# Kernel optimization log

Measured on AMD Instinct MI355X. Metric: run time of the kernel, lower is better.

## Reference

```python
import jax, jax.numpy as jnp
import numpy as np
import math

B, T, D, H = 2, 2048, 768, 12
ND = D // H  # head dim = 64


def precompute_freqs_cis(dim, end, theta=10000.0):
    freqs = 1.0 / (theta ** (jnp.arange(0, dim, 2, dtype=jnp.float32) / dim))  # [dim/2]
    t = jnp.arange(end, dtype=jnp.float32)
    freqs = jnp.outer(t, freqs)  # [end, dim/2]
    return jnp.cos(freqs), jnp.sin(freqs)


def apply_rotary_emb(q, k, cos, sin):
    # q, k: [b, t, h, nd]; cos/sin: [t, nd/2]
    def rot(x):
        xr, xi = x[..., 0::2], x[..., 1::2]  # even/odd interleaved split
        c = cos[None, :, None, :]
        s = sin[None, :, None, :]
        out_r = xr * c - xi * s
        out_i = xr * s + xi * c
        return jnp.stack([out_r, out_i], axis=-1).reshape(x.shape)
    return rot(q), rot(k)


def setup_inputs() -> dict:
    key = jax.random.key(0)
    ks = jax.random.split(key, 12)
    sc = 0.02
    q = jax.random.normal(ks[0], (B, T, D), dtype=jnp.float32)
    k = jax.random.normal(ks[1], (B, T, D), dtype=jnp.float32)
    v = jax.random.normal(ks[2], (B, T, D), dtype=jnp.float32)
    mask = jnp.tril(jnp.ones((T, T), dtype=jnp.int32))[None, None]  # causal [1,1,T,T]
    # weights stored as [d_in, d_out] (pre-transposed vs torch Linear)
    wq = jax.random.normal(ks[3], (D, D), dtype=jnp.float32) * sc
    bq = jax.random.normal(ks[4], (D,), dtype=jnp.float32) * sc
    wk = jax.random.normal(ks[5], (D, D), dtype=jnp.float32) * sc
    bk = jax.random.normal(ks[6], (D,), dtype=jnp.float32) * sc
    wv = jax.random.normal(ks[7], (D, D), dtype=jnp.float32) * sc
    bv = jax.random.normal(ks[8], (D,), dtype=jnp.float32) * sc
    wo = jax.random.normal(ks[9], (D, D), dtype=jnp.float32) * sc
    cos, sin = precompute_freqs_cis(ND, T)
    return {"q": q, "k": k, "v": v, "mask": mask, "wq": wq, "bq": bq,
            "wk": wk, "bk": bk, "wv": wv, "bv": bv, "wo": wo,
            "freqs_cos": cos, "freqs_sin": sin}


def reference(q, k, v, mask, wq, bq, wk, bk, wv, bv, wo, freqs_cos, freqs_sin):
    b, t, d = q.shape
    qh = (q @ wq + bq).reshape(b, t, H, ND)
    kh = (k @ wk + bk).reshape(b, t, H, ND)
    vh = (v @ wv + bv).reshape(b, t, H, ND).transpose(0, 2, 1, 3)  # [b,h,t,nd]
    qh, kh = apply_rotary_emb(qh, kh, freqs_cos[:t], freqs_sin[:t])
    qh = qh.transpose(0, 2, 1, 3)  # [b,h,t,nd]
    kh = kh.transpose(0, 2, 1, 3)
    attn = jnp.einsum('bhqd,bhkd->bhqk', qh, kh) / math.sqrt(ND)
    attn = jnp.where(mask == 0, jnp.float32(-jnp.inf), attn)
    probs = jax.nn.softmax(attn, axis=-1)
    out = jnp.einsum('bhqk,bhkd->bhqd', probs, vh)
    out = out.transpose(0, 2, 1, 3).reshape(b, t, d)
    return out @ wo
```

## Files before the change

### kernel.cpp

```cpp
#include <hip/hip_runtime.h>
#include <hip/hip_bf16.h>
#include <math.h>

#define BB 2
#define TT 2048
#define DD 768
#define HH 12
#define ND 64
#define MM (BB*TT)

typedef __attribute__((ext_vector_type(8))) short bf16x8;
typedef __attribute__((ext_vector_type(4))) float f32x4;
typedef __attribute__((ext_vector_type(16))) float f32x16;

__device__ __forceinline__ float bf2f(ushort u) {
    union { unsigned int i; float f; } v; v.i = ((unsigned int)u) << 16; return v.f;
}
__device__ __forceinline__ ushort f2bf(float f) {
    union { float f; unsigned int i; } v; v.f = f;
    unsigned int r = v.i + 0x7FFF + ((v.i >> 16) & 1);
    return (ushort)(r >> 16);
}

__device__ __forceinline__ void cp16(void* lds, const void* g) {
    __builtin_amdgcn_global_load_lds(
        (const __attribute__((address_space(1))) void*)g,
        (__attribute__((address_space(3))) void*)lds, 16, 0, 0);
}

__device__ __forceinline__ float fexp2(float x) {
    float r; asm("v_exp_f32 %0, %1" : "=v"(r) : "v"(x)); return r;
}
__device__ __forceinline__ unsigned int pk_bf16(float a, float b) {
    unsigned int r; asm("v_cvt_pk_bf16_f32 %0, %1, %2" : "=v"(r) : "v"(a), "v"(b)); return r;
}

__device__ __forceinline__ void plswap(unsigned int& a, unsigned int& b) {
#if __has_builtin(__builtin_amdgcn_permlane32_swap)
    auto r = __builtin_amdgcn_permlane32_swap(a, b, false, false);
    a = r[0]; b = r[1];
#else
    unsigned int sa = __shfl_xor((int)a, 32), sb = __shfl_xor((int)b, 32);
    bool hi = (threadIdx.x & 63) >= 32;
    unsigned int na = hi ? sb : a, nb = hi ? b : sa;
    a = na; b = nb;
#endif
}
__device__ __forceinline__ float partner32(float x, int hi) {
#if __has_builtin(__builtin_amdgcn_permlane32_swap)
    unsigned int u = __float_as_uint(x);
    auto r = __builtin_amdgcn_permlane32_swap(u, u, false, false);
    return __uint_as_float(hi ? r[0] : r[1]);
#else
    return __shfl_xor(x, 32);
#endif
}

#define QSCALE 0.18033688011112043f

__global__ void conv_x3(const float* __restrict__ x0, const float* __restrict__ x1,
                        const float* __restrict__ x2,
                        ushort* __restrict__ o0, ushort* __restrict__ o1,
                        ushort* __restrict__ o2)
{
    const float* x = blockIdx.z == 0 ? x0 : (blockIdx.z == 1 ? x1 : x2);
    ushort* o = blockIdx.z == 0 ? o0 : (blockIdx.z == 1 ? o1 : o2);
    int i = (blockIdx.x * 256 + threadIdx.x) * 4;
    if (i >= MM * DD) return;
    float4 v = *(const float4*)&x[i];
    ushort4 r;
    r.x = f2bf(v.x); r.y = f2bf(v.y); r.z = f2bf(v.z); r.w = f2bf(v.w);
    *(ushort4*)&o[i] = r;
}

__global__ __launch_bounds__(256) void conv_wT(const float* __restrict__ w0, const float* __restrict__ w1,
                        const float* __restrict__ w2, const float* __restrict__ w3,
                        ushort* __restrict__ o0, ushort* __restrict__ o1,
                        ushort* __restrict__ o2, ushort* __restrict__ o3)
{
    __shared__ ushort tile[64][72];
    const float* w = blockIdx.z == 0 ? w0 : blockIdx.z == 1 ? w1 : blockIdx.z == 2 ? w2 : w3;
    ushort* o = blockIdx.z == 0 ? o0 : blockIdx.z == 1 ? o1 : blockIdx.z == 2 ? o2 : o3;
    const int k0 = blockIdx.y * 64, n0 = blockIdx.x * 64;
    #pragma unroll
    for (int it = 0; it < 4; ++it) {
        int e = (threadIdx.x + it * 256) * 4;
        int r = e >> 6, c = e & 63;
        float4 v = *(const float4*)&w[(size_t)(k0 + r) * DD + n0 + c];
        tile[c + 0][r] = f2bf(v.x);
        tile[c + 1][r] = f2bf(v.y);
        tile[c + 2][r] = f2bf(v.z);
        tile[c + 3][r] = f2bf(v.w);
    }
    __syncthreads();
    #pragma unroll
    for (int it = 0; it < 4; ++it) {
        int e = (threadIdx.x + it * 256) * 4;
        int nr = e >> 6, kc = e & 63;
        ushort4 r4;
        r4.x = tile[nr][kc + 0];
        r4.y = tile[nr][kc + 1];
        r4.z = tile[nr][kc + 2];
        r4.w = tile[nr][kc + 3];
        *(ushort4*)&o[(size_t)(n0 + nr) * DD + k0 + kc] = r4;
    }
}

struct GArgs { const ushort* x; const ushort* wt; const float* bias; void* out;
               const float* cT; const float* sT; int rope; };

template<int MODE, int TM, int TN>
__global__ __launch_bounds__(256) void gemm_bf16(GArgs a0, GArgs a1, GArgs a2)
{
    constexpr int WM = TM / 2, WN = TN / 2;
    constexpr int MF = WM / 16, NF = WN / 16;
    constexpr int ABYTES = TM * 128;
    constexpr int BUFB = (TM + TN) * 128;
    constexpr int NPASS = BUFB / 4096;
    constexpr int NK = DD / 64;
    __shared__ __align__(16) ushort S[2][BUFB / 2];
    GArgs ga = (blockIdx.z == 0) ? a0 : (blockIdx.z == 1 ? a1 : a2);
    const int tid = threadIdx.x;
    const int w = tid >> 6, l = tid & 63;
    const int wr = w >> 1, wc = w & 1;
    const int n0 = blockIdx.x * TN, m0 = blockIdx.y * TM;

    f32x4 acc[MF][NF] = {};

    auto stage = [&](int buf, int k0) {
        #pragma unroll
        for (int it = 0; it < NPASS; ++it) {
            const int ob = it * 4096 + w * 1024;
            const int o = ob + l * 16;
            if (ob < ABYTES) {
                const int row = o >> 7, inner = o & 127;
                cp16((char*)&S[buf][0] + ob,
                     (const char*)ga.x + (size_t)(m0 + row) * (DD * 2) + k0 * 2 +
                     (inner ^ ((row & 7) << 4)));
            } else {
                const int o2 = o - ABYTES;
                const int row = o2 >> 7, inner = o2 & 127;
                cp16((char*)&S[buf][0] + ob,
                     (const char*)ga.wt + (size_t)(n0 + row) * (DD * 2) + k0 * 2 +
                     (inner ^ ((row & 7) << 4)));
            }
        }
    };

    stage(0, 0);
    __syncthreads();
    const int lq = l >> 4, lr = l & 15;
    for (int t = 0; t < NK; ++t) {
        const int cur = t & 1;
        if (t + 1 < NK) stage(cur ^ 1, (t + 1) * 64);
        const char* ab = (const char*)&S[cur][0];
        #pragma unroll
        for (int kc = 0; kc < 2; ++kc) {
            const int kb = kc * 64 + lq * 16;
            bf16x8 af[MF], bfr[NF];
            #pragma unroll
            for (int i = 0; i < MF; ++i) {
                const int row = WM * wr + 16 * i + lr;
                af[i] = *(const bf16x8*)(ab + row * 128 + (kb ^ ((row & 7) << 4)));
            }
            #pragma unroll
            for (int j = 0; j < NF; ++j) {
                const int row = WN * wc + 16 * j + lr;
                bfr[j] = *(const bf16x8*)(ab + ABYTES + row * 128 + (kb ^ ((row & 7) << 4)));
            }
            __builtin_amdgcn_s_setprio(1);
            #pragma unroll
            for (int i = 0; i < MF; ++i)
                #pragma unroll
                for (int j = 0; j < NF; ++j)
                    acc[i][j] = __builtin_amdgcn_mfma_f32_16x16x32_bf16(af[i], bfr[j], acc[i][j], 0, 0, 0);
            __builtin_amdgcn_s_setprio(0);
        }
        __syncthreads();
    }

    #pragma unroll
    for (int i = 0; i < MF; ++i) {
        #pragma unroll
        for (int j = 0; j < NF; ++j) {
            #pragma unroll
            for (int r = 0; r < 4; ++r) {
                const int m = m0 + WM * wr + 16 * i + (l >> 4) * 4 + r;
                const int n = n0 + WN * wc + 16 * j + (l & 15);
                float v = acc[i][j][r];
                if (MODE == 0) {
                    v += ga.bias[n];
                    const int tt = m & 2047;
                    if (ga.rope) {
                        const int d = n & 63;
                        const float c = ga.cT[tt * 32 + (d >> 1)];
                        const float s = ga.sT[tt * 32 + (d >> 1)];
                        const float pv = __shfl_xor(v, 1);
                        v = (n & 1) ? (pv * s + v * c) : (v * c - pv * s);
                        if (ga.rope == 2) v *= QSCALE;
                    }
                    const int b = m >> 11;
                    const int h = n >> 6, d = n & 63;
                    ((ushort*)ga.out)[((size_t)(b * HH + h) * TT + tt) * ND + d] = f2bf(v);
                } else {
                    ((float*)ga.out)[(size_t)m * DD + n] = v;
                }
            }
        }
    }
}

__global__ __launch_bounds__(256) void transpose_v(const ushort* __restrict__ Vh,
                                                   ushort* __restrict__ VhT)
{
    __shared__ ushort tile[64][72];
    const int t0 = blockIdx.x * 64, bh = blockIdx.y;
    const ushort* src = Vh + ((size_t)bh * TT + t0) * ND;
    #pragma unroll
    for (int it = 0; it < 4; ++it) {
        int e = (threadIdx.x + it * 256) * 4;
        int r = e >> 6, c = e & 63;
        ushort4 v = *(const ushort4*)&src[r * ND + c];
        tile[r][c + 0] = v.x; tile[r][c + 1] = v.y;
        tile[r][c + 2] = v.z; tile[r][c + 3] = v.w;
    }
    __syncthreads();
    #pragma unroll
    for (int it = 0; it < 4; ++it) {
        int e = (threadIdx.x + it * 256) * 4;
        int d = e >> 6, tc = e & 63;
        ushort4 r4;
        r4.x = tile[tc + 0][d]; r4.y = tile[tc + 1][d];
        r4.z = tile[tc + 2][d]; r4.w = tile[tc + 3][d];
        *(ushort4*)&VhT[((size_t)bh * ND + d) * TT + t0 + tc] = r4;
    }
}

#define NQB (TT/128)
#define NBH (BB*HH)
#define NTASK (NQB*NBH)
#define NCU 256

__global__ __launch_bounds__(512) void attn_mfma4(const ushort* __restrict__ Qh,
                                                  const ushort* __restrict__ Kh,
                                                  const ushort* __restrict__ VhT,
                                                  ushort* __restrict__ Op)
{
    __shared__ __align__(16) ushort Ks[2][2][4096];
    __shared__ __align__(16) ushort Vs[2][2][4096];
    const int tid = threadIdx.x;
    const int w = tid >> 6, l = tid & 63;
    const int lq = l & 31, hi = l >> 5;
    const int qs = w & 3;
    const int kvh = w >> 2;

    const int n = blockIdx.x;
    const int r_ = (n < NCU) ? n : (NTASK - 1 + NCU - n);
    const int qblk = (NQB - 1) - r_ / NBH;
    const int bh = r_ % NBH;

    const int q0 = qblk * 128;
    const int q0w = q0 + qs * 32;
    const int qg = q0w + lq;
    const int ntH = qblk + 1;
    const int kvbase = kvh * ntH * 64;

    const ushort* Qg = Qh + ((size_t)bh * TT + q0w) * ND;
    const ushort* Kg = Kh + (size_t)bh * TT * ND;
    const ushort* Vg = VhT + (size_t)bh * ND * TT;

    bf16x8 qf[4];
    #pragma unroll
    for (int ks = 0; ks < 4; ++ks)
        qf[ks] = *(const bf16x8*)((const char*)Qg + lq * 128 + ks * 32 + hi * 16);

    auto stageKV = [&](int buf, int kv0) {
        #pragma unroll
        for (int it = 0; it < 2; ++it) {
            int o = it * 4096 + qs * 1024 + l * 16;
            int row = o >> 7, inner = o & 127;
            int swz = inner ^ ((row & 7) << 4);
            cp16((char*)&Ks[kvh][buf][0] + it * 4096 + qs * 1024,
                 (const char*)Kg + (size_t)(kv0 + row) * 128 + swz);
            cp16((char*)&Vs[kvh][buf][0] + it * 4096 + qs * 1024,
                 (const char*)Vg + (size_t)row * (TT * 2) + kv0 * 2 + swz);
        }
    };

    float m = -1e30f, lsum = 0.f;
    f32x16 o0 = {}, o1 = {};

    stageKV(0, kvbase);
    __syncthreads();
    for (int t = 0; t < ntH; ++t) {
        const int cur = t & 1;
        if (t + 1 < ntH) stageKV(cur ^ 1, kvbase + (t + 1) * 64);
        const char* kb = (const char*)&Ks[kvh][cur][0];
        const char* vb = (const char*)&Vs[kvh][cur][0];
        const int kvt = kvbase + t * 64;

        if (kvt <= q0w + 31) {
            const bool have1 = (kvt + 32 <= q0w + 31);

            f32x16 st0 = {}, st1 = {};
            __builtin_amdgcn_s_setprio(1);
            #pragma unroll
            for (int ks = 0; ks < 4; ++ks) {
                bf16x8 kf = *(const bf16x8*)(kb + lq * 128 +
                                             ((ks * 32 + hi * 16) ^ ((lq & 7) << 4)));
                st0 = __builtin_amdgcn_mfma_f32_32x32x16_bf16(kf, qf[ks], st0, 0, 0, 0);
            }
            if (have1) {
                #pragma unroll
                for (int ks = 0; ks < 4; ++ks) {
                    bf16x8 kf = *(const bf16x8*)(kb + (32 + lq) * 128 +
                                                 ((ks * 32 + hi * 16) ^ ((lq & 7) << 4)));
                    st1 = __builtin_amdgcn_mfma_f32_32x32x16_bf16(kf, qf[ks], st1, 0, 0, 0);
                }
            }
            __builtin_amdgcn_s_setprio(0);

            float tm = -1e30f;
            if (kvt + 31 > q0w) {
                #pragma unroll
                for (int r = 0; r < 16; ++r) {
                    const int kvg = kvt + (r & 3) + 8 * (r >> 2) + 4 * hi;
                    float x = (kvg <= qg) ? st0[r] : -1e30f;
                    st0[r] = x;
                    tm = fmaxf(tm, x);
                }
            } else {
                #pragma unroll
                for (int r = 0; r < 16; ++r) tm = fmaxf(tm, st0[r]);
            }
            if (have1) {
                if (kvt + 63 > q0w) {
                    #pragma unroll
                    for (int r = 0; r < 16; ++r) {
                        const int kvg = kvt + 32 + (r & 3) + 8 * (r >> 2) + 4 * hi;
                        float x = (kvg <= qg) ? st1[r] : -1e30f;
                        st1[r] = x;
                        tm = fmaxf(tm, x);
                    }
                } else {
                    #pragma unroll
                    for (int r = 0; r < 16; ++r) tm = fmaxf(tm, st1[r]);
                }
            }
            tm = fmaxf(tm, partner32(tm, hi));

            const bool defer = __all(tm <= m + 11.5f);
            float alpha = 1.f;
            if (!defer) {
                const float nm = fmaxf(m, tm);
                alpha = fexp2(m - nm);
                m = nm;
            }

            float ps[16];
            unsigned int pkA[8], pkB[8];
            #pragma unroll
            for (int i = 0; i < 8; ++i) {
                const float p0 = fexp2(st0[2 * i + 0] - m);
                const float p1 = fexp2(st0[2 * i + 1] - m);
                pkA[i] = pk_bf16(p0, p1);
                ps[i] = p0 + p1;
            }
            if (have1) {
                #pragma unroll
                for (int i = 0; i < 8; ++i) {
                    const float p0 = fexp2(st1[2 * i + 0] - m);
                    const float p1 = fexp2(st1[2 * i + 1] - m);
                    pkB[i] = pk_bf16(p0, p1);
                    ps[8 + i] = p0 + p1;
                }
            } else {
                #pragma unroll
                for (int i = 0; i < 8; ++i) { pkB[i] = 0; ps[8 + i] = 0.f; }
            }
            const float t0s = (ps[0] + ps[1]) + (ps[2] + ps[3]);
            const float t1s = (ps[4] + ps[5]) + (ps[6] + ps[7]);
            const float t2s = (ps[8] + ps[9]) + (ps[10] + ps[11]);
            const float t3s = (ps[12] + ps[13]) + (ps[14] + ps[15]);
            float rs = (t0s + t1s) + (t2s + t3s);
            rs += partner32(rs, hi);
            lsum = lsum * alpha + rs;

            plswap(pkA[0], pkA[2]); plswap(pkA[1], pkA[3]);
            plswap(pkA[4], pkA[6]); plswap(pkA[5], pkA[7]);
            if (have1) {
                plswap(pkB[0], pkB[2]); plswap(pkB[1], pkB[3]);
                plswap(pkB[4], pkB[6]); plswap(pkB[5], pkB[7]);
            }
            union { unsigned int u[4]; bf16x8 v; } pa0, pa1, pa2, pa3;
            pa0.u[0] = pkA[0]; pa0.u[1] = pkA[1]; pa0.u[2] = pkA[2]; pa0.u[3] = pkA[3];
            pa1.u[0] = pkA[4]; pa1.u[1] = pkA[5]; pa1.u[2] = pkA[6]; pa1.u[3] = pkA[7];
            pa2.u[0] = pkB[0]; pa2.u[1] = pkB[1]; pa2.u[2] = pkB[2]; pa2.u[3] = pkB[3];
            pa3.u[0] = pkB[4]; pa3.u[1] = pkB[5]; pa3.u[2] = pkB[6]; pa3.u[3] = pkB[7];

            if (!defer) {
                #pragma unroll
                for (int r = 0; r < 16; ++r) { o0[r] *= alpha; o1[r] *= alpha; }
            }

            __builtin_amdgcn_s_setprio(1);
            #pragma unroll
            for (int sl = 0; sl < 2; ++sl) {
                const bf16x8 pf = sl == 0 ? pa0.v : pa1.v;
                const int cb = sl * 32 + hi * 16;
                bf16x8 va = *(const bf16x8*)(vb + lq * 128 + (cb ^ ((lq & 7) << 4)));
                bf16x8 vc = *(const bf16x8*)(vb + (lq + 32) * 128 + (cb ^ ((lq & 7) << 4)));
                o0 = __builtin_amdgcn_mfma_f32_32x32x16_bf16(va, pf, o0, 0, 0, 0);
                o1 = __builtin_amdgcn_mfma_f32_32x32x16_bf16(vc, pf, o1, 0, 0, 0);
            }
            if (have1) {
                #pragma unroll
                for (int sl = 0; sl < 2; ++sl) {
                    const bf16x8 pf = sl == 0 ? pa2.v : pa3.v;
                    const int cb = 64 + sl * 32 + hi * 16;
                    bf16x8 va = *(const bf16x8*)(vb + lq * 128 + (cb ^ ((lq & 7) << 4)));
                    bf16x8 vc = *(const bf16x8*)(vb + (lq + 32) * 128 + (cb ^ ((lq & 7) << 4)));
                    o0 = __builtin_amdgcn_mfma_f32_32x32x16_bf16(va, pf, o0, 0, 0, 0);
                    o1 = __builtin_amdgcn_mfma_f32_32x32x16_bf16(vc, pf, o1, 0, 0, 0);
                }
            }
            __builtin_amdgcn_s_setprio(0);
        }
        __syncthreads();
    }

    float* xO  = (float*)&Ks[0][0][0];
    float* xML = (float*)&Vs[0][0][0];
    if (kvh == 1) {
        float* dst = xO + qs * 2048;
        #pragma unroll
        for (int r = 0; r < 16; ++r) {
            dst[r * 64 + l] = o0[r];
            dst[(r + 16) * 64 + l] = o1[r];
        }
        if (hi == 0) { xML[qs * 64 + lq] = m; xML[qs * 64 + 32 + lq] = lsum; }
    }
    __syncthreads();
    if (kvh == 0) {
        const float* src = xO + qs * 2048;
        const float m1 = xML[qs * 64 + lq];
        const float l1 = xML[qs * 64 + 32 + lq];
        const float ms = fmaxf(m, m1);
        const float a0 = fexp2(m - ms), a1 = fexp2(m1 - ms);
        const float inv = 1.0f / (lsum * a0 + l1 * a1);
        const int b = bh / HH, h = bh % HH;
        ushort* dst = Op + ((size_t)(b * TT + qg)) * DD + h * ND;
        #pragma unroll
        for (int g = 0; g < 4; ++g) {
            ushort4 w0, w1;
            w0.x = f2bf((o0[4 * g + 0] * a0 + src[(4 * g + 0) * 64 + l] * a1) * inv);
            w0.y = f2bf((o0[4 * g + 1] * a0 + src[(4 * g + 1) * 64 + l] * a1) * inv);
            w0.z = f2bf((o0[4 * g + 2] * a0 + src[(4 * g + 2) * 64 + l] * a1) * inv);
            w0.w = f2bf((o0[4 * g + 3] * a0 + src[(4 * g + 3) * 64 + l] * a1) * inv);
            *(ushort4*)&dst[8 * g + 4 * hi] = w0;
            w1.x = f2bf((o1[4 * g + 0] * a0 + src[(16 + 4 * g + 0) * 64 + l] * a1) * inv);
            w1.y = f2bf((o1[4 * g + 1] * a0 + src[(16 + 4 * g + 1) * 64 + l] * a1) * inv);
            w1.z = f2bf((o1[4 * g + 2] * a0 + src[(16 + 4 * g + 2) * 64 + l] * a1) * inv);
            w1.w = f2bf((o1[4 * g + 3] * a0 + src[(16 + 4 * g + 3) * 64 + l] * a1) * inv);
            *(ushort4*)&dst[32 + 8 * g + 4 * hi] = w1;
        }
    }
}

extern "C" void kernel_launch(void* const* d_in, const int* in_sizes, int n_in,
                              void* d_out, int out_size, void* d_ws, size_t ws_size,
                              hipStream_t stream)
{
    const float* q  = (const float*)d_in[0];
    const float* k  = (const float*)d_in[1];
    const float* v  = (const float*)d_in[2];
    const float* wq = (const float*)d_in[4];
    const float* bq = (const float*)d_in[5];
    const float* wk = (const float*)d_in[6];
    const float* bk = (const float*)d_in[7];
    const float* wv = (const float*)d_in[8];
    const float* bv = (const float*)d_in[9];
    const float* wo = (const float*)d_in[10];
    const float* fc = (const float*)d_in[11];
    const float* fs = (const float*)d_in[12];
    float* out = (float*)d_out;

    ushort* qB  = (ushort*)d_ws;
    ushort* kB  = qB  + (size_t)MM * DD;
    ushort* vB  = kB  + (size_t)MM * DD;
    ushort* wqT = vB  + (size_t)MM * DD;
    ushort* wkT = wqT + (size_t)DD * DD;
    ushort* wvT = wkT + (size_t)DD * DD;
    ushort* woT = wvT + (size_t)DD * DD;
    ushort* Qh  = woT + (size_t)DD * DD;
    ushort* Kh  = Qh  + (size_t)MM * DD;
    ushort* Vh  = Kh  + (size_t)MM * DD;
    ushort* VhT = kB;
    ushort* Op  = qB;

    conv_x3<<<dim3(MM * DD / 4 / 256, 1, 3), 256, 0, stream>>>(q, k, v, qB, kB, vB);
    conv_wT<<<dim3(DD / 64, DD / 64, 4), 256, 0, stream>>>(wq, wk, wv, wo, wqT, wkT, wvT, woT);

    GArgs aq{qB, wqT, bq, (void*)Qh, fc, fs, 2};
    GArgs ak{kB, wkT, bk, (void*)Kh, fc, fs, 1};
    GArgs av{vB, wvT, bv, (void*)Vh, nullptr, nullptr, 0};
    gemm_bf16<0, 128, 64><<<dim3(DD / 64, MM / 128, 3), 256, 0, stream>>>(aq, ak, av);

    transpose_v<<<dim3(TT / 64, BB * HH), 256, 0, stream>>>(Vh, VhT);

    attn_mfma4<<<dim3(NTASK), 512, 0, stream>>>(Qh, Kh, VhT, Op);

    GArgs ao{Op, woT, nullptr, (void*)out, nullptr, nullptr, 0};
    gemm_bf16<1, 64, 64><<<dim3(DD / 64, MM / 64, 1), 256, 0, stream>>>(ao, ao, ao);
}
```

Measured before the change: 105.1 us.

## Fuse V transpose into projection GEMM epilogue and merge conversion kernels

The V projection GEMM now stages its bias-added bf16 tile in shared memory and writes it directly in the transposed [b,h,d,t] layout the attention kernel reads. This removes the separate transpose_v kernel and its extra global round trip. The input and weight conversion kernels are merged into one grid-strided launch to cut launch overhead. The costs are an extra LDS pass and a barrier in the V epilogue, plus idle blocks in the weight slices of the merged grid.

Result: faster. 99.23 us (-5.6%).

```diff
diff --git a/kernel.cpp b/kernel.cpp
--- a/kernel.cpp
+++ b/kernel.cpp
@@ -58,51 +58,55 @@
 
 #define QSCALE 0.18033688011112043f
 
-__global__ void conv_x3(const float* __restrict__ x0, const float* __restrict__ x1,
-                        const float* __restrict__ x2,
-                        ushort* __restrict__ o0, ushort* __restrict__ o1,
-                        ushort* __restrict__ o2)
+__global__ __launch_bounds__(256) void conv_all(
+    const float* __restrict__ x0, const float* __restrict__ x1, const float* __restrict__ x2,
+    ushort* __restrict__ o0, ushort* __restrict__ o1, ushort* __restrict__ o2,
+    const float* __restrict__ w0, const float* __restrict__ w1,
+    const float* __restrict__ w2, const float* __restrict__ w3,
+    ushort* __restrict__ t0, ushort* __restrict__ t1,
+    ushort* __restrict__ t2, ushort* __restrict__ t3)
 {
-    const float* x = blockIdx.z == 0 ? x0 : (blockIdx.z == 1 ? x1 : x2);
-    ushort* o = blockIdx.z == 0 ? o0 : (blockIdx.z == 1 ? o1 : o2);
-    int i = (blockIdx.x * 256 + threadIdx.x) * 4;
-    if (i >= MM * DD) return;
-    float4 v = *(const float4*)&x[i];
-    ushort4 r;
-    r.x = f2bf(v.x); r.y = f2bf(v.y); r.z = f2bf(v.z); r.w = f2bf(v.w);
-    *(ushort4*)&o[i] = r;
-}
-
-__global__ __launch_bounds__(256) void conv_wT(const float* __restrict__ w0, const float* __restrict__ w1,
-                        const float* __restrict__ w2, const float* __restrict__ w3,
-                        ushort* __restrict__ o0, ushort* __restrict__ o1,
-                        ushort* __restrict__ o2, ushort* __restrict__ o3)
-{
-    __shared__ ushort tile[64][72];
-    const float* w = blockIdx.z == 0 ? w0 : blockIdx.z == 1 ? w1 : blockIdx.z == 2 ? w2 : w3;
-    ushort* o = blockIdx.z == 0 ? o0 : blockIdx.z == 1 ? o1 : blockIdx.z == 2 ? o2 : o3;
-    const int k0 = blockIdx.y * 64, n0 = blockIdx.x * 64;
-    #pragma unroll
-    for (int it = 0; it < 4; ++it) {
-        int e = (threadIdx.x + it * 256) * 4;
-        int r = e >> 6, c = e & 63;
-        float4 v = *(const float4*)&w[(size_t)(k0 + r) * DD + n0 + c];
-        tile[c + 0][r] = f2bf(v.x);
-        tile[c + 1][r] = f2bf(v.y);
-        tile[c + 2][r] = f2bf(v.z);
-        tile[c + 3][r] = f2bf(v.w);
-    }
-    __syncthreads();
-    #pragma unroll
-    for (int it = 0; it < 4; ++it) {
-        int e = (threadIdx.x + it * 256) * 4;
-        int nr = e >> 6, kc = e & 63;
-        ushort4 r4;
-        r4.x = tile[nr][kc + 0];
-        r4.y = tile[nr][kc + 1];
-        r4.z = tile[nr][kc + 2];
-        r4.w = tile[nr][kc + 3];
-        *(ushort4*)&o[(size_t)(n0 + nr) * DD + k0 + kc] = r4;
+    const int z = blockIdx.z;
+    if (z < 3) {
+        const float* x = z == 0 ? x0 : (z == 1 ? x1 : x2);
+        ushort* o = z == 0 ? o0 : (z == 1 ? o1 : o2);
+        const int total4 = MM * DD / 4;
+        for (int i = blockIdx.x * 256 + threadIdx.x; i < total4; i += gridDim.x * 256) {
+            float4 v = *(const float4*)&x[i * 4];
+            ushort4 r;
+            r.x = f2bf(v.x); r.y = f2bf(v.y); r.z = f2bf(v.z); r.w = f2bf(v.w);
+            *(ushort4*)&o[i * 4] = r;
+        }
+    } else {
+        if (blockIdx.x >= (DD / 64) * (DD / 64)) return;
+        __shared__ ushort tile[64][72];
+        const int zz = z - 3;
+        const float* w = zz == 0 ? w0 : zz == 1 ? w1 : zz == 2 ? w2 : w3;
+        ushort* o = zz == 0 ? t0 : zz == 1 ? t1 : zz == 2 ? t2 : t3;
+        const int n0 = (blockIdx.x % (DD / 64)) * 64;
+        const int k0 = (blockIdx.x / (DD / 64)) * 64;
+        #pragma unroll
+        for (int it = 0; it < 4; ++it) {
+            int e = (threadIdx.x + it * 256) * 4;
+            int r = e >> 6, c = e & 63;
+            float4 v = *(const float4*)&w[(size_t)(k0 + r) * DD + n0 + c];
+            tile[c + 0][r] = f2bf(v.x);
+            tile[c + 1][r] = f2bf(v.y);
+            tile[c + 2][r] = f2bf(v.z);
+            tile[c + 3][r] = f2bf(v.w);
+        }
+        __syncthreads();
+        #pragma unroll
+        for (int it = 0; it < 4; ++it) {
+            int e = (threadIdx.x + it * 256) * 4;
+            int nr = e >> 6, kc = e & 63;
+            ushort4 r4;
+            r4.x = tile[nr][kc + 0];
+            r4.y = tile[nr][kc + 1];
+            r4.z = tile[nr][kc + 2];
+            r4.w = tile[nr][kc + 3];
+            *(ushort4*)&o[(size_t)(n0 + nr) * DD + k0 + kc] = r4;
+        }
     }
 }
 
@@ -179,6 +183,33 @@
         __syncthreads();
     }
 
+    if (MODE == 0 && ga.rope == -1) {
+        ushort* tl = (ushort*)&S[0][0];
+        #pragma unroll
+        for (int i = 0; i < MF; ++i) {
+            #pragma unroll
+            for (int j = 0; j < NF; ++j) {
+                #pragma unroll
+                for (int r = 0; r < 4; ++r) {
+                    const int ml = WM * wr + 16 * i + (l >> 4) * 4 + r;
+                    const int nl = WN * wc + 16 * j + (l & 15);
+                    tl[nl * (TM + 8) + ml] = f2bf(acc[i][j][r] + ga.bias[n0 + nl]);
+                }
+            }
+        }
+        __syncthreads();
+        const int b = m0 >> 11, t0b = m0 & 2047, h = n0 >> 6;
+        ushort* base = (ushort*)ga.out + ((size_t)(b * HH + h) * ND) * TT + t0b;
+        #pragma unroll
+        for (int it = 0; it < TM * TN / (256 * 8); ++it) {
+            const int slot = tid + it * 256;
+            const int d = slot / (TM / 8), c = (slot % (TM / 8)) * 8;
+            bf16x8 v = *(const bf16x8*)&tl[d * (TM + 8) + c];
+            *(bf16x8*)&base[(size_t)d * TT + c] = v;
+        }
+        return;
+    }
+
     #pragma unroll
     for (int i = 0; i < MF; ++i) {
         #pragma unroll
@@ -191,7 +222,7 @@
                 if (MODE == 0) {
                     v += ga.bias[n];
                     const int tt = m & 2047;
-                    if (ga.rope) {
+                    if (ga.rope > 0) {
                         const int d = n & 63;
                         const float c = ga.cT[tt * 32 + (d >> 1)];
                         const float s = ga.sT[tt * 32 + (d >> 1)];
@@ -207,32 +238,6 @@
                 }
             }
         }
-    }
-}
-
-__global__ __launch_bounds__(256) void transpose_v(const ushort* __restrict__ Vh,
-                                                   ushort* __restrict__ VhT)
-{
-    __shared__ ushort tile[64][72];
-    const int t0 = blockIdx.x * 64, bh = blockIdx.y;
-    const ushort* src = Vh + ((size_t)bh * TT + t0) * ND;
-    #pragma unroll
-    for (int it = 0; it < 4; ++it) {
-        int e = (threadIdx.x + it * 256) * 4;
-        int r = e >> 6, c = e & 63;
-        ushort4 v = *(const ushort4*)&src[r * ND + c];
-        tile[r][c + 0] = v.x; tile[r][c + 1] = v.y;
-        tile[r][c + 2] = v.z; tile[r][c + 3] = v.w;
-    }
-    __syncthreads();
-    #pragma unroll
-    for (int it = 0; it < 4; ++it) {
-        int e = (threadIdx.x + it * 256) * 4;
-        int d = e >> 6, tc = e & 63;
-        ushort4 r4;
-        r4.x = tile[tc + 0][d]; r4.y = tile[tc + 1][d];
-        r4.z = tile[tc + 2][d]; r4.w = tile[tc + 3][d];
-        *(ushort4*)&VhT[((size_t)bh * ND + d) * TT + t0 + tc] = r4;
     }
 }
 
@@ -494,19 +499,16 @@
     ushort* woT = wvT + (size_t)DD * DD;
     ushort* Qh  = woT + (size_t)DD * DD;
     ushort* Kh  = Qh  + (size_t)MM * DD;
-    ushort* Vh  = Kh  + (size_t)MM * DD;
-    ushort* VhT = kB;
+    ushort* VhT = Kh  + (size_t)MM * DD;
     ushort* Op  = qB;
 
-    conv_x3<<<dim3(MM * DD / 4 / 256, 1, 3), 256, 0, stream>>>(q, k, v, qB, kB, vB);
-    conv_wT<<<dim3(DD / 64, DD / 64, 4), 256, 0, stream>>>(wq, wk, wv, wo, wqT, wkT, wvT, woT);
+    conv_all<<<dim3(2048, 1, 7), 256, 0, stream>>>(q, k, v, qB, kB, vB,
+                                                   wq, wk, wv, wo, wqT, wkT, wvT, woT);
 
     GArgs aq{qB, wqT, bq, (void*)Qh, fc, fs, 2};
     GArgs ak{kB, wkT, bk, (void*)Kh, fc, fs, 1};
-    GArgs av{vB, wvT, bv, (void*)Vh, nullptr, nullptr, 0};
+    GArgs av{vB, wvT, bv, (void*)VhT, nullptr, nullptr, -1};
     gemm_bf16<0, 128, 64><<<dim3(DD / 64, MM / 128, 3), 256, 0, stream>>>(aq, ak, av);
-
-    transpose_v<<<dim3(TT / 64, BB * HH), 256, 0, stream>>>(Vh, VhT);
 
     attn_mfma4<<<dim3(NTASK), 512, 0, stream>>>(Qh, Kh, VhT, Op);
 
```
